# Optimization experiments

Measured on AMD Instinct MI355X. Metric: run time of the kernel, lower is better.

## Reference

```python
import jax, jax.numpy as jnp
import numpy as np

N = 50000
H = 4
C = 32  # hidden_channels // heads
NEG_SLOPE = 0.2


def gat_layer(x, W, a_src, a_dst, b, src, dst):
    # x: [N, F_in]; W: [F_in, H*C]; a_src/a_dst: [H, C]; b: [H*C]
    h = (x @ W).reshape(N, H, C)                      # [N, H, C]
    alpha_src = jnp.sum(h * a_src, axis=-1)           # [N, H]
    alpha_dst = jnp.sum(h * a_dst, axis=-1)           # [N, H]
    e = jax.nn.leaky_relu(alpha_src[src] + alpha_dst[dst], NEG_SLOPE)  # [E, H]
    # softmax over incoming edges per destination node (stable)
    m = jax.ops.segment_max(e, dst, num_segments=N)   # [N, H]
    p = jnp.exp(e - m[dst])                           # [E, H]
    s = jax.ops.segment_sum(p, dst, num_segments=N)   # [N, H]
    alpha = p / s[dst]                                # [E, H]
    msg = h[src] * alpha[:, :, None]                  # [E, H, C]
    out = jax.ops.segment_sum(msg, dst, num_segments=N)  # [N, H, C]
    return out.reshape(N, H * C) + b


def setup_inputs() -> dict:
    key = jax.random.key(0)
    ks = jax.random.split(key, 12)
    E = 1600000
    x = jax.random.normal(ks[0], (N, 128), dtype=jnp.float32)
    edge_index = jax.random.randint(ks[1], (2, E), 0, N, dtype=jnp.int32)
    s = 0.08
    return {
        "x": x,
        "edge_index": edge_index,
        "W1": jax.random.normal(ks[2], (128, H * C), dtype=jnp.float32) * s,
        "a_src1": jax.random.normal(ks[3], (H, C), dtype=jnp.float32) * s,
        "a_dst1": jax.random.normal(ks[4], (H, C), dtype=jnp.float32) * s,
        "b1": jnp.zeros((H * C,), dtype=jnp.float32),
        "W2": jax.random.normal(ks[5], (H * C, H * C), dtype=jnp.float32) * s,
        "a_src2": jax.random.normal(ks[6], (H, C), dtype=jnp.float32) * s,
        "a_dst2": jax.random.normal(ks[7], (H, C), dtype=jnp.float32) * s,
        "b2": jnp.zeros((H * C,), dtype=jnp.float32),
    }


def reference(x, edge_index, W1, a_src1, a_dst1, b1, W2, a_src2, a_dst2, b2):
    # PyG GATConv default add_self_loops=True: append (i -> i) edges
    loops = jnp.arange(N, dtype=edge_index.dtype)
    src = jnp.concatenate([edge_index[0], loops])
    dst = jnp.concatenate([edge_index[1], loops])
    # layer 1 + ELU (dropout is identity in eval mode)
    h = gat_layer(x, W1, a_src1, a_dst1, b1, src, dst)
    h = jax.nn.elu(h)
    # layer 2 + ELU
    h = gat_layer(h, W2, a_src2, a_dst2, b2, src, dst)
    h = jax.nn.elu(h)
    return h
```

## Files before the change

### kernel.cpp

```cpp
#include <hip/hip_runtime.h>
#include <hip/hip_bf16.h>

typedef _Float16 half8 __attribute__((ext_vector_type(8)));
typedef float f32x4 __attribute__((ext_vector_type(4)));

static __device__ __forceinline__ float bf2f_lo(unsigned u) {
    return __uint_as_float(u << 16);
}
static __device__ __forceinline__ float bf2f_hi(unsigned u) {
    return __uint_as_float(u & 0xffff0000u);
}
static __device__ __forceinline__ unsigned f2bf_rne_bits(float f) {
    unsigned u = __float_as_uint(f);
    return u + 0x7fffu + ((u >> 16) & 1u);
}
static __device__ __forceinline__ unsigned pack_bf2(float a, float b) {
    return (f2bf_rne_bits(a) >> 16) | (f2bf_rne_bits(b) & 0xffff0000u);
}
static __device__ __forceinline__ float pfun(float e) {
    e = fmaxf(e, 0.2f * e);
    return __expf(e);
}

#define CHUNK 4096

__global__ void kb_zero(int* bucketCount, int NBK) {
    int i = blockIdx.x * 256 + threadIdx.x;
    if (i < NBK) bucketCount[i] = 0;
}

__global__ void kb_count(const int* __restrict__ dst, int* bucketCount,
                         int E, int T, int NBK) {
    __shared__ int cnt[256];
    const int tid = threadIdx.x;
    const int beg = blockIdx.x * CHUNK;
    const int end = min(beg + CHUNK, T);
    cnt[tid] = 0;
    __syncthreads();
    for (int i = beg + tid; i < end; i += 256) {
        int d = (i < E) ? dst[i] : (i - E);
        atomicAdd(&cnt[d >> 8], 1);
    }
    __syncthreads();
    if (tid < NBK && cnt[tid] > 0) atomicAdd(&bucketCount[tid], cnt[tid]);
}

__global__ void kb_scan(const int* __restrict__ bucketCount, int* bucketBase,
                        int* bucketCursor, int* row_ptr, int NBK, int N, int total) {
    __shared__ int sm[256];
    const int tid = threadIdx.x;
    int v = (tid < NBK) ? bucketCount[tid] : 0;
    sm[tid] = v;
    __syncthreads();
    for (int off = 1; off < 256; off <<= 1) {
        int t = (tid >= off) ? sm[tid - off] : 0;
        __syncthreads();
        sm[tid] += t;
        __syncthreads();
    }
    if (tid < NBK) {
        int ex = sm[tid] - v;
        bucketBase[tid] = ex;
        bucketCursor[tid] = ex;
    }
    if (tid == 0) {
        bucketBase[NBK] = total;
        row_ptr[N] = total;
    }
}

__global__ void kb_place(const int* __restrict__ src, const int* __restrict__ dst,
                         int* bucketCursor, unsigned* __restrict__ barr,
                         int E, int T, int NBK) {
    __shared__ int cnt[256];
    __shared__ int wb[256];
    const int tid = threadIdx.x;
    const int beg = blockIdx.x * CHUNK;
    const int end = min(beg + CHUNK, T);
    cnt[tid] = 0;
    __syncthreads();
    for (int i = beg + tid; i < end; i += 256) {
        int d = (i < E) ? dst[i] : (i - E);
        atomicAdd(&cnt[d >> 8], 1);
    }
    __syncthreads();
    if (tid < NBK) {
        int c = cnt[tid];
        wb[tid] = (c > 0) ? atomicAdd(&bucketCursor[tid], c) : 0;
    }
    __syncthreads();
    cnt[tid] = 0;
    __syncthreads();
    for (int i = beg + tid; i < end; i += 256) {
        int s, d;
        if (i < E) { s = src[i]; d = dst[i]; }
        else       { s = i - E;  d = s; }
        int g = d >> 8;
        unsigned pk = (unsigned)s | ((unsigned)(d & 255) << 16);
        int r = atomicAdd(&cnt[g], 1);
        barr[wb[g] + r] = pk;
    }
}

__global__ void kb_csr(const unsigned* __restrict__ barr, const int* __restrict__ bucketBase,
                       int* __restrict__ row_ptr, int* __restrict__ col, int N) {
    __shared__ int cnt[256];
    __shared__ int sm[256];
    __shared__ int cur[256];
    const int tid = threadIdx.x;
    const int b = blockIdx.x;
    const int beg = bucketBase[b];
    const int end = bucketBase[b + 1];
    cnt[tid] = 0;
    __syncthreads();
    for (int i = beg + tid; i < end; i += 256)
        atomicAdd(&cnt[barr[i] >> 16], 1);
    __syncthreads();
    int v = cnt[tid];
    sm[tid] = v;
    __syncthreads();
    for (int off = 1; off < 256; off <<= 1) {
        int t = (tid >= off) ? sm[tid - off] : 0;
        __syncthreads();
        sm[tid] += t;
        __syncthreads();
    }
    int ex = sm[tid] - v;
    int n = b * 256 + tid;
    if (n < N) row_ptr[n] = beg + ex;
    cur[tid] = beg + ex;
    __syncthreads();
    for (int i = beg + tid; i < end; i += 256) {
        unsigned p = barr[i];
        int pos = atomicAdd(&cur[p >> 16], 1);
        col[pos] = (int)(p & 0xFFFFu);
    }
}

__launch_bounds__(256)
__global__ void k_gemm(const float* __restrict__ A, const float* __restrict__ W,
                       const float* __restrict__ a_src, const float* __restrict__ a_dst,
                       unsigned* __restrict__ Hout,
                       float* __restrict__ asrc_o, float* __restrict__ adst_o,
                       int nrows, int ntiles) {
    __shared__ _Float16 Wt[128 * 136];
    const int tid = threadIdx.x;
    for (int idx = tid; idx < 128 * 128 / 4; idx += 256) {
        int k = idx >> 5;
        int c4 = (idx & 31) * 4;
        float4 v = *(const float4*)&W[(size_t)k * 128 + c4];
        Wt[(c4 + 0) * 136 + k] = (_Float16)v.x;
        Wt[(c4 + 1) * 136 + k] = (_Float16)v.y;
        Wt[(c4 + 2) * 136 + k] = (_Float16)v.z;
        Wt[(c4 + 3) * 136 + k] = (_Float16)v.w;
    }
    __syncthreads();
    const int lane = tid & 63;
    const int m = lane & 15, quad = lane >> 4;

    half8 wf[4][8];
#pragma unroll
    for (int ks = 0; ks < 4; ++ks)
#pragma unroll
        for (int ct = 0; ct < 8; ++ct)
            wf[ks][ct] = *(half8*)&Wt[(ct * 16 + m) * 136 + ks * 32 + quad * 8];

    const int wv = (blockIdx.x * 256 + tid) >> 6;
    const int nwaves = gridDim.x * 4;
    for (int t = wv; t < ntiles; t += nwaves) {
        const int row = t * 16 + m;
        const int rc = min(row, nrows - 1);
        const float* ap = A + (size_t)rc * 128;
        f32x4 acc[8];
#pragma unroll
        for (int ct = 0; ct < 8; ++ct) acc[ct] = (f32x4){0.f, 0.f, 0.f, 0.f};
#pragma unroll
        for (int ks = 0; ks < 4; ++ks) {
            float4 x0 = *(const float4*)&ap[ks * 32 + quad * 8];
            float4 x1 = *(const float4*)&ap[ks * 32 + quad * 8 + 4];
            half8 af;
            af[0] = (_Float16)x0.x; af[1] = (_Float16)x0.y;
            af[2] = (_Float16)x0.z; af[3] = (_Float16)x0.w;
            af[4] = (_Float16)x1.x; af[5] = (_Float16)x1.y;
            af[6] = (_Float16)x1.z; af[7] = (_Float16)x1.w;
#pragma unroll
            for (int ct = 0; ct < 8; ++ct)
                acc[ct] = __builtin_amdgcn_mfma_f32_16x16x32_f16(wf[ks][ct], af, acc[ct], 0, 0, 0);
        }
        if (row < nrows) {
#pragma unroll
            for (int ct = 0; ct < 8; ++ct) {
                uint2 o;
                o.x = pack_bf2(acc[ct][0], acc[ct][1]);
                o.y = pack_bf2(acc[ct][2], acc[ct][3]);
                *(uint2*)&Hout[(size_t)row * 64 + ct * 8 + quad * 2] = o;
            }
        }
        float ps[4] = {0.f, 0.f, 0.f, 0.f}, pd[4] = {0.f, 0.f, 0.f, 0.f};
#pragma unroll
        for (int ct = 0; ct < 8; ++ct) {
            int hh = ct >> 1;
#pragma unroll
            for (int r = 0; r < 4; ++r) {
                int c = ct * 16 + quad * 4 + r;
                ps[hh] += acc[ct][r] * a_src[c];
                pd[hh] += acc[ct][r] * a_dst[c];
            }
        }
#pragma unroll
        for (int hh = 0; hh < 4; ++hh) {
            ps[hh] += __shfl_xor(ps[hh], 16); ps[hh] += __shfl_xor(ps[hh], 32);
            pd[hh] += __shfl_xor(pd[hh], 16); pd[hh] += __shfl_xor(pd[hh], 32);
        }
        if (row < nrows) {
            asrc_o[(size_t)row * 4 + quad] = ps[quad];
            adst_o[(size_t)row * 4 + quad] = pd[quad];
        }
    }
}

#define BAT 16
__launch_bounds__(256)
__global__ void k_aggr(const unsigned* __restrict__ h,
                       const float* __restrict__ asrc, const float* __restrict__ adst,
                       const float* __restrict__ bias,
                       const int* __restrict__ row_ptr, const int* __restrict__ col,
                       float* __restrict__ out, int N) {
    const int lane = threadIdx.x & 63;
    const int d = blockIdx.x * 4 + (threadIdx.x >> 6);
    if (d >= N) return;
    const int eb  = lane >> 2;
    const int hp  = lane & 3;
    const int hdc = lane >> 4;
    const float adv = adst[(size_t)d * 4 + hp];
    const int beg = row_ptr[d];
    const int end = row_ptr[d + 1];

    float ac0 = 0.f, ac1 = 0.f, sp = 0.f;
    int cv = 0;
    { int idx = beg + eb; if (idx < end) cv = col[idx]; }

    for (int j = beg; j < end; j += BAT) {
        int cvn = 0;
        { int idx = j + BAT + eb; if (idx < end) cvn = col[idx]; }

        float a = asrc[(size_t)(unsigned)cv * 4 + hp];
        float p = (j + eb < end) ? pfun(a + adv) : 0.f;
        sp += p;

        unsigned u[BAT];
#pragma unroll
        for (int k = 0; k < BAT; ++k) {
            int sk = __builtin_amdgcn_readlane(cv, 4 * k);
            u[k] = h[(size_t)(unsigned)sk * 64 + lane];
        }
#pragma unroll
        for (int k = 0; k < BAT; ++k) {
            float pk = __shfl(p, 4 * k + hdc);
            ac0 += pk * bf2f_lo(u[k]);
            ac1 += pk * bf2f_hi(u[k]);
        }
        cv = cvn;
    }

    sp += __shfl_xor(sp, 4);
    sp += __shfl_xor(sp, 8);
    sp += __shfl_xor(sp, 16);
    sp += __shfl_xor(sp, 32);
    float spv = __shfl(sp, hdc);
    float inv = 1.f / spv;

    int c = 2 * lane;
    float v0 = ac0 * inv + bias[c];
    float v1 = ac1 * inv + bias[c + 1];
    v0 = (v0 > 0.f) ? v0 : (__expf(v0) - 1.f);
    v1 = (v1 > 0.f) ? v1 : (__expf(v1) - 1.f);
    *(float2*)&out[(size_t)d * 128 + c] = make_float2(v0, v1);
}

extern "C" void kernel_launch(void* const* d_in, const int* in_sizes, int n_in,
                              void* d_out, int out_size, void* d_ws, size_t ws_size,
                              hipStream_t stream) {
    const float* x      = (const float*)d_in[0];
    const int*   ei     = (const int*)d_in[1];
    const float* W1     = (const float*)d_in[2];
    const float* a_src1 = (const float*)d_in[3];
    const float* a_dst1 = (const float*)d_in[4];
    const float* b1     = (const float*)d_in[5];
    const float* W2     = (const float*)d_in[6];
    const float* a_src2 = (const float*)d_in[7];
    const float* a_dst2 = (const float*)d_in[8];
    const float* b2     = (const float*)d_in[9];

    const int N = in_sizes[0] / 128;
    const int E = in_sizes[1] / 2;
    const int T = E + N;
    const int NBK = (N + 255) / 256;
    const int* src = ei;
    const int* dst = ei + E;

    char* w = (char*)d_ws;
    auto alloc = [&](size_t bytes) -> char* {
        char* p = w;
        w += (bytes + 255) & ~(size_t)255;
        return p;
    };
    unsigned* h_bf    = (unsigned*)alloc((size_t)N * 64 * 4);
    float*    o1      = (float*)alloc((size_t)N * 128 * 4);
    float*    asrc    = (float*)alloc((size_t)N * 4 * 4);
    float*    adst    = (float*)alloc((size_t)N * 4 * 4);
    int*      row_ptr = (int*)alloc((size_t)(N + 1) * 4);
    int*      col     = (int*)alloc((size_t)T * 4);
    int*      bCount  = (int*)alloc((size_t)NBK * 4);
    int*      bBase   = (int*)alloc((size_t)(NBK + 1) * 4);
    int*      bCursor = (int*)alloc((size_t)NBK * 4);
    unsigned* barr    = (unsigned*)o1;
    (void)ws_size; (void)n_in; (void)out_size;

    const int PB = (T + CHUNK - 1) / CHUNK;

    hipLaunchKernelGGL(kb_zero, dim3((NBK + 255) / 256), dim3(256), 0, stream, bCount, NBK);
    hipLaunchKernelGGL(kb_count, dim3(PB), dim3(256), 0, stream, dst, bCount, E, T, NBK);
    hipLaunchKernelGGL(kb_scan, dim3(1), dim3(256), 0, stream, bCount, bBase, bCursor, row_ptr, NBK, N, T);
    hipLaunchKernelGGL(kb_place, dim3(PB), dim3(256), 0, stream, src, dst, bCursor, barr, E, T, NBK);
    hipLaunchKernelGGL(kb_csr, dim3(NBK), dim3(256), 0, stream, barr, bBase, row_ptr, col, N);

    const int ntiles = (N + 15) / 16;
    const int GB = 512;
    const int AB = (N + 3) / 4;

    hipLaunchKernelGGL(k_gemm, dim3(GB), dim3(256), 0, stream, x, W1, a_src1, a_dst1, h_bf, asrc, adst, N, ntiles);
    hipLaunchKernelGGL(k_aggr, dim3(AB), dim3(256), 0, stream, h_bf, asrc, adst, b1, row_ptr, col, o1, N);
    hipLaunchKernelGGL(k_gemm, dim3(GB), dim3(256), 0, stream, o1, W2, a_src2, a_dst2, h_bf, asrc, adst, N, ntiles);
    hipLaunchKernelGGL(k_aggr, dim3(AB), dim3(256), 0, stream, h_bf, asrc, adst, b2, row_ptr, col, (float*)d_out, N);
}
```

Baseline: 307.0 us.

## Fuse bucket scan into count, store layer-1 output as fp16, prefetch aggregation rows

```diff
diff --git a/kernel.cpp b/kernel.cpp
--- a/kernel.cpp
+++ b/kernel.cpp
@@ -21,17 +21,20 @@
     e = fmaxf(e, 0.2f * e);
     return __expf(e);
 }
+static __device__ __forceinline__ unsigned pack_h2(float a, float b) {
+    union { _Float16 f[2]; unsigned u; } pk;
+    pk.f[0] = (_Float16)a; pk.f[1] = (_Float16)b;
+    return pk.u;
+}
 
 #define CHUNK 4096
 
-__global__ void kb_zero(int* bucketCount, int NBK) {
-    int i = blockIdx.x * 256 + threadIdx.x;
-    if (i < NBK) bucketCount[i] = 0;
-}
-
-__global__ void kb_count(const int* __restrict__ dst, int* bucketCount,
-                         int E, int T, int NBK) {
+__global__ void kb_count(const int* __restrict__ dst, int* bucketCount, int* ticket,
+                         int* bucketBase, int* bucketCursor, int* row_ptr,
+                         int E, int T, int NBK, int N, int nblocks) {
     __shared__ int cnt[256];
+    __shared__ int sm[256];
+    __shared__ int isLast;
     const int tid = threadIdx.x;
     const int beg = blockIdx.x * CHUNK;
     const int end = min(beg + CHUNK, T);
@@ -43,13 +46,12 @@
     }
     __syncthreads();
     if (tid < NBK && cnt[tid] > 0) atomicAdd(&bucketCount[tid], cnt[tid]);
-}
-
-__global__ void kb_scan(const int* __restrict__ bucketCount, int* bucketBase,
-                        int* bucketCursor, int* row_ptr, int NBK, int N, int total) {
-    __shared__ int sm[256];
-    const int tid = threadIdx.x;
-    int v = (tid < NBK) ? bucketCount[tid] : 0;
+    __threadfence();
+    __syncthreads();
+    if (tid == 0) isLast = (atomicAdd(ticket, 1) == nblocks - 1);
+    __syncthreads();
+    if (!isLast) return;
+    int v = (tid < NBK) ? atomicAdd(&bucketCount[tid], 0) : 0;
     sm[tid] = v;
     __syncthreads();
     for (int off = 1; off < 256; off <<= 1) {
@@ -64,8 +66,8 @@
         bucketCursor[tid] = ex;
     }
     if (tid == 0) {
-        bucketBase[NBK] = total;
-        row_ptr[N] = total;
+        bucketBase[NBK] = T;
+        row_ptr[N] = T;
     }
 }
 
@@ -137,22 +139,23 @@
     }
 }
 
+template <bool HALF_IN>
 __launch_bounds__(256)
-__global__ void k_gemm(const float* __restrict__ A, const float* __restrict__ W,
+__global__ void k_gemm(const void* __restrict__ Ain, const float* __restrict__ W,
                        const float* __restrict__ a_src, const float* __restrict__ a_dst,
                        unsigned* __restrict__ Hout,
                        float* __restrict__ asrc_o, float* __restrict__ adst_o,
                        int nrows, int ntiles) {
-    __shared__ _Float16 Wt[128 * 136];
+    __shared__ _Float16 Wt[128 * 140];
     const int tid = threadIdx.x;
     for (int idx = tid; idx < 128 * 128 / 4; idx += 256) {
         int k = idx >> 5;
         int c4 = (idx & 31) * 4;
         float4 v = *(const float4*)&W[(size_t)k * 128 + c4];
-        Wt[(c4 + 0) * 136 + k] = (_Float16)v.x;
-        Wt[(c4 + 1) * 136 + k] = (_Float16)v.y;
-        Wt[(c4 + 2) * 136 + k] = (_Float16)v.z;
-        Wt[(c4 + 3) * 136 + k] = (_Float16)v.w;
+        Wt[(c4 + 0) * 140 + k] = (_Float16)v.x;
+        Wt[(c4 + 1) * 140 + k] = (_Float16)v.y;
+        Wt[(c4 + 2) * 140 + k] = (_Float16)v.z;
+        Wt[(c4 + 3) * 140 + k] = (_Float16)v.w;
     }
     __syncthreads();
     const int lane = tid & 63;
@@ -163,26 +166,31 @@
     for (int ks = 0; ks < 4; ++ks)
 #pragma unroll
         for (int ct = 0; ct < 8; ++ct)
-            wf[ks][ct] = *(half8*)&Wt[(ct * 16 + m) * 136 + ks * 32 + quad * 8];
+            wf[ks][ct] = *(half8*)&Wt[(ct * 16 + m) * 140 + ks * 32 + quad * 8];
 
     const int wv = (blockIdx.x * 256 + tid) >> 6;
     const int nwaves = gridDim.x * 4;
     for (int t = wv; t < ntiles; t += nwaves) {
         const int row = t * 16 + m;
         const int rc = min(row, nrows - 1);
-        const float* ap = A + (size_t)rc * 128;
         f32x4 acc[8];
 #pragma unroll
         for (int ct = 0; ct < 8; ++ct) acc[ct] = (f32x4){0.f, 0.f, 0.f, 0.f};
 #pragma unroll
         for (int ks = 0; ks < 4; ++ks) {
-            float4 x0 = *(const float4*)&ap[ks * 32 + quad * 8];
-            float4 x1 = *(const float4*)&ap[ks * 32 + quad * 8 + 4];
             half8 af;
-            af[0] = (_Float16)x0.x; af[1] = (_Float16)x0.y;
-            af[2] = (_Float16)x0.z; af[3] = (_Float16)x0.w;
-            af[4] = (_Float16)x1.x; af[5] = (_Float16)x1.y;
-            af[6] = (_Float16)x1.z; af[7] = (_Float16)x1.w;
+            if (HALF_IN) {
+                const _Float16* ap = (const _Float16*)Ain + (size_t)rc * 128;
+                af = *(const half8*)&ap[ks * 32 + quad * 8];
+            } else {
+                const float* ap = (const float*)Ain + (size_t)rc * 128;
+                float4 x0 = *(const float4*)&ap[ks * 32 + quad * 8];
+                float4 x1 = *(const float4*)&ap[ks * 32 + quad * 8 + 4];
+                af[0] = (_Float16)x0.x; af[1] = (_Float16)x0.y;
+                af[2] = (_Float16)x0.z; af[3] = (_Float16)x0.w;
+                af[4] = (_Float16)x1.x; af[5] = (_Float16)x1.y;
+                af[6] = (_Float16)x1.z; af[7] = (_Float16)x1.w;
+            }
 #pragma unroll
             for (int ct = 0; ct < 8; ++ct)
                 acc[ct] = __builtin_amdgcn_mfma_f32_16x16x32_f16(wf[ks][ct], af, acc[ct], 0, 0, 0);
@@ -225,7 +233,7 @@
                        const float* __restrict__ asrc, const float* __restrict__ adst,
                        const float* __restrict__ bias,
                        const int* __restrict__ row_ptr, const int* __restrict__ col,
-                       float* __restrict__ out, int N) {
+                       float* __restrict__ out_f, unsigned* __restrict__ out_h, int N) {
     const int lane = threadIdx.x & 63;
     const int d = blockIdx.x * 4 + (threadIdx.x >> 6);
     if (d >= N) return;
@@ -237,8 +245,15 @@
     const int end = row_ptr[d + 1];
 
     float ac0 = 0.f, ac1 = 0.f, sp = 0.f;
+
     int cv = 0;
     { int idx = beg + eb; if (idx < end) cv = col[idx]; }
+    unsigned ucur[BAT];
+#pragma unroll
+    for (int k = 0; k < BAT; ++k) {
+        int sk = __builtin_amdgcn_readlane(cv, 4 * k);
+        ucur[k] = h[(size_t)(unsigned)sk * 64 + lane];
+    }
 
     for (int j = beg; j < end; j += BAT) {
         int cvn = 0;
@@ -248,18 +263,22 @@
         float p = (j + eb < end) ? pfun(a + adv) : 0.f;
         sp += p;
 
-        unsigned u[BAT];
-#pragma unroll
-        for (int k = 0; k < BAT; ++k) {
-            int sk = __builtin_amdgcn_readlane(cv, 4 * k);
-            u[k] = h[(size_t)(unsigned)sk * 64 + lane];
+        unsigned unext[BAT];
+        if (j + BAT < end) {
+#pragma unroll
+            for (int k = 0; k < BAT; ++k) {
+                int sk = __builtin_amdgcn_readlane(cvn, 4 * k);
+                unext[k] = h[(size_t)(unsigned)sk * 64 + lane];
+            }
         }
 #pragma unroll
         for (int k = 0; k < BAT; ++k) {
             float pk = __shfl(p, 4 * k + hdc);
-            ac0 += pk * bf2f_lo(u[k]);
-            ac1 += pk * bf2f_hi(u[k]);
-        }
+            ac0 += pk * bf2f_lo(ucur[k]);
+            ac1 += pk * bf2f_hi(ucur[k]);
+        }
+#pragma unroll
+        for (int k = 0; k < BAT; ++k) ucur[k] = unext[k];
         cv = cvn;
     }
 
@@ -275,7 +294,11 @@
     float v1 = ac1 * inv + bias[c + 1];
     v0 = (v0 > 0.f) ? v0 : (__expf(v0) - 1.f);
     v1 = (v1 > 0.f) ? v1 : (__expf(v1) - 1.f);
-    *(float2*)&out[(size_t)d * 128 + c] = make_float2(v0, v1);
+    if (out_h) {
+        out_h[(size_t)d * 64 + lane] = pack_h2(v0, v1);
+    } else {
+        *(float2*)&out_f[(size_t)d * 128 + c] = make_float2(v0, v1);
+    }
 }
 
 extern "C" void kernel_launch(void* const* d_in, const int* in_sizes, int n_in,
@@ -306,22 +329,23 @@
         return p;
     };
     unsigned* h_bf    = (unsigned*)alloc((size_t)N * 64 * 4);
-    float*    o1      = (float*)alloc((size_t)N * 128 * 4);
+    unsigned* o1h     = (unsigned*)alloc((size_t)N * 64 * 4);
     float*    asrc    = (float*)alloc((size_t)N * 4 * 4);
     float*    adst    = (float*)alloc((size_t)N * 4 * 4);
     int*      row_ptr = (int*)alloc((size_t)(N + 1) * 4);
     int*      col     = (int*)alloc((size_t)T * 4);
-    int*      bCount  = (int*)alloc((size_t)NBK * 4);
+    unsigned* barr    = (unsigned*)alloc((size_t)T * 4);
+    int*      bCount  = (int*)alloc((size_t)(NBK + 1) * 4);
     int*      bBase   = (int*)alloc((size_t)(NBK + 1) * 4);
     int*      bCursor = (int*)alloc((size_t)NBK * 4);
-    unsigned* barr    = (unsigned*)o1;
+    int*      ticket  = bCount + NBK;
     (void)ws_size; (void)n_in; (void)out_size;
 
     const int PB = (T + CHUNK - 1) / CHUNK;
 
-    hipLaunchKernelGGL(kb_zero, dim3((NBK + 255) / 256), dim3(256), 0, stream, bCount, NBK);
-    hipLaunchKernelGGL(kb_count, dim3(PB), dim3(256), 0, stream, dst, bCount, E, T, NBK);
-    hipLaunchKernelGGL(kb_scan, dim3(1), dim3(256), 0, stream, bCount, bBase, bCursor, row_ptr, NBK, N, T);
+    hipMemsetAsync(bCount, 0, (size_t)(NBK + 1) * 4, stream);
+    hipLaunchKernelGGL(kb_count, dim3(PB), dim3(256), 0, stream,
+                       dst, bCount, ticket, bBase, bCursor, row_ptr, E, T, NBK, N, PB);
     hipLaunchKernelGGL(kb_place, dim3(PB), dim3(256), 0, stream, src, dst, bCursor, barr, E, T, NBK);
     hipLaunchKernelGGL(kb_csr, dim3(NBK), dim3(256), 0, stream, barr, bBase, row_ptr, col, N);
 
@@ -329,8 +353,12 @@
     const int GB = 512;
     const int AB = (N + 3) / 4;
 
-    hipLaunchKernelGGL(k_gemm, dim3(GB), dim3(256), 0, stream, x, W1, a_src1, a_dst1, h_bf, asrc, adst, N, ntiles);
-    hipLaunchKernelGGL(k_aggr, dim3(AB), dim3(256), 0, stream, h_bf, asrc, adst, b1, row_ptr, col, o1, N);
-    hipLaunchKernelGGL(k_gemm, dim3(GB), dim3(256), 0, stream, o1, W2, a_src2, a_dst2, h_bf, asrc, adst, N, ntiles);
-    hipLaunchKernelGGL(k_aggr, dim3(AB), dim3(256), 0, stream, h_bf, asrc, adst, b2, row_ptr, col, (float*)d_out, N);
-}
+    hipLaunchKernelGGL((k_gemm<false>), dim3(GB), dim3(256), 0, stream,
+                       (const void*)x, W1, a_src1, a_dst1, h_bf, asrc, adst, N, ntiles);
+    hipLaunchKernelGGL(k_aggr, dim3(AB), dim3(256), 0, stream,
+                       h_bf, asrc, adst, b1, row_ptr, col, (float*)nullptr, o1h, N);
+    hipLaunchKernelGGL((k_gemm<true>), dim3(GB), dim3(256), 0, stream,
+                       (const void*)o1h, W2, a_src2, a_dst2, h_bf, asrc, adst, N, ntiles);
+    hipLaunchKernelGGL(k_aggr, dim3(AB), dim3(256), 0, stream,
+                       h_bf, asrc, adst, b2, row_ptr, col, (float*)d_out, (unsigned*)nullptr, N);
+}
```

Measured after the change: 340.9 us. +11.0%, slower.
